# Kernel optimization log

Measured on AMD Instinct MI355X. Metric: run time of the kernel, lower is better.

The kernel has to match this reference:

```python
import jax, jax.numpy as jnp
import numpy as np

B, N, D = 4, 2048, 1024
HEAD_DIMS = 128
NUM_HEADS = 8
PROJ = HEAD_DIMS * NUM_HEADS  # 1024


def setup_inputs() -> dict:
    key = jax.random.key(0)
    ks = jax.random.split(key, 5)
    # Weights stored as (in, out); xavier-normal-like scale
    def xavier(k, fan_in, fan_out):
        std = (2.0 / (fan_in + fan_out)) ** 0.5
        return jax.random.normal(k, (fan_in, fan_out), dtype=jnp.float32) * std
    return {
        "x": jax.random.normal(ks[0], (B, N, D), dtype=jnp.float32),
        "Wq": xavier(ks[1], D, PROJ),
        "Wk": xavier(ks[2], D, PROJ),
        "Wv": xavier(ks[3], D, PROJ),
        "Wo": xavier(ks[4], PROJ, PROJ),
    }


def reference(x, Wq, Wk, Wv, Wo):
    b, n, d = x.shape
    # QKV projections, split into heads: (b, h, n, hd)
    def split_heads(z):
        return z.reshape(b, n, NUM_HEADS, HEAD_DIMS).transpose(0, 2, 1, 3)
    q = split_heads(x @ Wq)
    k = split_heads(x @ Wk)
    v = split_heads(x @ Wv)
    scale = 1.0 / jnp.sqrt(jnp.float32(HEAD_DIMS))
    logits = jnp.einsum("bhqd,bhkd->bhqk", q, k) * scale
    weights = jax.nn.softmax(logits, axis=-1)
    out = jnp.einsum("bhqk,bhkd->bhqd", weights, v)
    out = out.transpose(0, 2, 1, 3).reshape(b, n, PROJ)
    return out @ Wo
```

## Files before the change

### kernel.cpp

```cpp
#include <hip/hip_runtime.h>
#include <hip/hip_bf16.h>


typedef __attribute__((ext_vector_type(8))) short short8;
typedef __attribute__((ext_vector_type(4))) short short4v;
typedef __attribute__((ext_vector_type(4))) float floatx4;
typedef __attribute__((ext_vector_type(8))) _Float16 half8;

#define MFMA_F16(a, b, c) __builtin_amdgcn_mfma_f32_16x16x32_f16( \
    __builtin_bit_cast(half8, (a)), __builtin_bit_cast(half8, (b)), (c), 0, 0, 0)

static constexpr int BATCH  = 4;
static constexpr int NHEADS = 8;
static constexpr int SEQ    = 2048;
static constexpr int HD     = 128;
static constexpr int DMODEL = 1024;
static constexpr int MROWS  = BATCH * SEQ;
static constexpr int NQKV   = 3 * DMODEL;

#define QSCALE2 0.12752283786512624f

static __device__ __forceinline__ short f16bits(float v) {
    return __builtin_bit_cast(short, (_Float16)v);
}

template <typename T>
static __device__ __forceinline__ short8 load8_f16(const T* p) {
    if constexpr (sizeof(T) == 2) {
        return *(const short8*)p;
    } else {
        const float4 f0 = *(const float4*)p;
        const float4 f1 = *(const float4*)(p + 4);
        short8 r;
        r[0] = f16bits(f0.x); r[1] = f16bits(f0.y);
        r[2] = f16bits(f0.z); r[3] = f16bits(f0.w);
        r[4] = f16bits(f1.x); r[5] = f16bits(f1.y);
        r[6] = f16bits(f1.z); r[7] = f16bits(f1.w);
        return r;
    }
}

static __device__ __forceinline__ void storeC(float* C, size_t idx, float v) {
    C[idx] = v;
}
static __device__ __forceinline__ void storeC(_Float16* C, size_t idx, float v) {
    C[idx] = (_Float16)v;
}

static __device__ __forceinline__ void gload16(const short* g, short* l) {
    __builtin_amdgcn_global_load_lds(
        (const __attribute__((address_space(1))) void*)g,
        (__attribute__((address_space(3))) void*)l, 16, 0, 0);
}

__global__ __launch_bounds__(256)
void prep(const float* __restrict__ x, short* __restrict__ xb,
          const float* __restrict__ W0, const float* __restrict__ W1,
          const float* __restrict__ W2, const float* __restrict__ W3,
          short* __restrict__ Wt, int K, int N)
{
    __shared__ short T[32][33];
    const int z = blockIdx.z;
    if (z >= 4) {
        const size_t chunk = ((size_t)(z - 4) * 1024 + blockIdx.y * 32 + blockIdx.x);
        const size_t i = (chunk * 256 + threadIdx.x) * 8;
        *(short8*)&xb[i] = load8_f16(&x[i]);
        return;
    }
    const float* W = (z == 0) ? W0 : (z == 1) ? W1 : (z == 2) ? W2 : W3;
    short* Wtz = Wt + (size_t)z * K * N;

    const int n0 = blockIdx.x * 32, k0 = blockIdx.y * 32;
    const int r = threadIdx.x >> 3, c4 = (threadIdx.x & 7) * 4;

    const float4 v = *(const float4*)&W[(size_t)(k0 + r) * N + n0 + c4];
    T[r][c4 + 0] = f16bits(v.x);
    T[r][c4 + 1] = f16bits(v.y);
    T[r][c4 + 2] = f16bits(v.z);
    T[r][c4 + 3] = f16bits(v.w);
    __syncthreads();

    short4v o;
    o[0] = T[c4 + 0][r]; o[1] = T[c4 + 1][r];
    o[2] = T[c4 + 2][r]; o[3] = T[c4 + 3][r];
    *(short4v*)&Wtz[(size_t)(n0 + r) * K + k0 + c4] = o;
}

__global__ __launch_bounds__(256)
void convx(const float* __restrict__ x, short* __restrict__ xb)
{
    const size_t i = ((size_t)blockIdx.x * 256 + threadIdx.x) * 8;
    *(short8*)&xb[i] = load8_f16(&x[i]);
}

__global__ __launch_bounds__(256)
void transpose_v(const short* __restrict__ V, short* __restrict__ Vt)
{
    __shared__ short T[64][72];
    const int s0 = blockIdx.x * 64;
    const int d0 = blockIdx.y * 64;
    const int bh = blockIdx.z;
    const short* Vi = V  + (size_t)bh * SEQ * HD;
    short*       Vo = Vt + (size_t)bh * HD * SEQ;

    const int r = threadIdx.x >> 3;
    const int c = threadIdx.x & 7;

    *(short8*)&T[r][c * 8]      = *(const short8*)&Vi[(size_t)(s0 + r) * HD + d0 + c * 8];
    *(short8*)&T[r + 32][c * 8] = *(const short8*)&Vi[(size_t)(s0 + r + 32) * HD + d0 + c * 8];
    __syncthreads();

    short8 o0, o1;
    #pragma unroll
    for (int j = 0; j < 8; ++j) {
        o0[j] = T[c * 8 + j][r];
        o1[j] = T[c * 8 + j][r + 32];
    }
    *(short8*)&Vo[(size_t)(d0 + r) * SEQ + s0 + c * 8]      = o0;
    *(short8*)&Vo[(size_t)(d0 + r + 32) * SEQ + s0 + c * 8] = o1;
}

template <typename OutT, bool QKV>
__global__ __launch_bounds__(256)
void gemm128(const short* __restrict__ A, const short* __restrict__ Bt,
             OutT* __restrict__ C, int M, int N, int K, size_t qkvStride)
{
    __shared__ __align__(16) short As[128 * 64];
    __shared__ __align__(16) short Bs[128 * 64];

    const int tid  = threadIdx.x;
    const int lane = tid & 63;
    const int w    = tid >> 6;
    const int quad = lane >> 4;
    const int l16  = lane & 15;

    const int m0 = blockIdx.x * 128;
    const int n0 = blockIdx.y * 128;
    const int wm = (w >> 1) * 64;
    const int wn = (w & 1) * 64;

    floatx4 acc[4][4] = {};

    const int srow   = tid >> 3;
    const int schunk = (tid & 7) ^ (srow & 7);
    const short* aG = A  + (size_t)(m0 + srow) * K + schunk * 8;
    const short* bG = Bt + (size_t)(n0 + srow) * K + schunk * 8;
    short* aL = As + tid * 8;
    short* bL = Bs + tid * 8;

    const int fsw = l16 & 7;

    for (int k0 = 0; k0 < K; k0 += 64) {
        __syncthreads();
        #pragma unroll
        for (int r = 0; r < 4; ++r) {
            gload16(aG + k0 + (size_t)(r * 32) * K, aL + r * 2048);
            gload16(bG + k0 + (size_t)(r * 32) * K, bL + r * 2048);
        }
        __syncthreads();

        #pragma unroll
        for (int kk = 0; kk < 2; ++kk) {
            short8 af[4], bf[4];
            #pragma unroll
            for (int mi = 0; mi < 4; ++mi)
                af[mi] = *(short8*)&As[(wm + mi * 16 + l16) * 64 +
                                       (((kk * 4 + quad) ^ fsw) * 8)];
            #pragma unroll
            for (int ni = 0; ni < 4; ++ni)
                bf[ni] = *(short8*)&Bs[(wn + ni * 16 + l16) * 64 +
                                       (((kk * 4 + quad) ^ fsw) * 8)];

            #pragma unroll
            for (int mi = 0; mi < 4; ++mi)
                #pragma unroll
                for (int ni = 0; ni < 4; ++ni)
                    acc[mi][ni] = MFMA_F16(af[mi], bf[ni], acc[mi][ni]);
        }
    }

    #pragma unroll
    for (int mi = 0; mi < 4; ++mi)
        #pragma unroll
        for (int ni = 0; ni < 4; ++ni)
            #pragma unroll
            for (int r = 0; r < 4; ++r) {
                const int m = m0 + wm + mi * 16 + quad * 4 + r;
                const int n = n0 + wn + ni * 16 + l16;
                float v = acc[mi][ni][r];
                if constexpr (QKV) {
                    const int qkv = n >> 10, rem = n & 1023;
                    const int h = rem >> 7, d = rem & 127;
                    const int b = m >> 11, s = m & 2047;
                    if (qkv == 0) v *= QSCALE2;
                    storeC(C, (size_t)qkv * qkvStride +
                              (((size_t)b * NHEADS + h) * SEQ + s) * HD + d, v);
                } else {
                    storeC(C, (size_t)m * N + n, v);
                }
            }
}

__global__ __launch_bounds__(256)
void attn_flash10(const short* __restrict__ Q, const short* __restrict__ K,
                  const short* __restrict__ Vt, _Float16* __restrict__ O)
{
    __shared__ __align__(16) short Ks[2][32 * 128];
    __shared__ __align__(16) short Vs[2][128 * 32];
    __shared__ __align__(16) short Plds[4][16 * 40];

    const int tid  = threadIdx.x;
    const int lane = tid & 63;
    const int w    = tid >> 6;
    const int quad = lane >> 4;
    const int l16  = lane & 15;

    const int h  = blockIdx.x & 7;
    const int qi = blockIdx.x >> 3;
    const int b  = blockIdx.y;
    const int q0 = qi * 64;

    const short* Qh  = Q  + (((size_t)b * NHEADS + h) * SEQ) * HD;
    const short* Kh  = K  + (((size_t)b * NHEADS + h) * SEQ) * HD;
    const short* Vth = Vt + (((size_t)b * NHEADS + h) * HD) * SEQ;

    const int qrow = q0 + w * 16 + l16;
    short8 qf[4];
    #pragma unroll
    for (int c = 0; c < 4; ++c)
        qf[c] = *(const short8*)&Qh[(size_t)qrow * HD + c * 32 + quad * 8];

    const int kr0 = tid >> 4, kc0 = tid & 15;
    const int kr1 = kr0 + 16;
    const short* kGa = Kh + (size_t)kr0 * HD + ((kc0 ^ (kr0 & 15)) * 8);
    const short* kGb = Kh + (size_t)kr1 * HD + ((kc0 ^ (kr1 & 15)) * 8);
    const int vr0 = tid >> 2, vp0 = tid & 3;
    const short* vGa = Vth + (size_t)vr0 * SEQ + ((vp0 ^ ((vr0 >> 1) & 3)) * 8);
    const short* vGb = Vth + (size_t)(vr0 + 64) * SEQ + ((vp0 ^ ((vr0 >> 1) & 3)) * 8);

    floatx4 acc[8] = {};
    floatx4 acc9 = {};

    short8 ones;
    #pragma unroll
    for (int j = 0; j < 8; ++j) ones[j] = 0x3C00;

    const int fswV = (l16 >> 1) & 3;
    short* Pw = &Plds[w][0];

    auto STAGE = [&](short* kDst, short* vDst, int tile) {
        const size_t ko = (size_t)tile * 32 * HD;
        const size_t vo = (size_t)tile * 32;
        gload16(kGa + ko, kDst + tid * 8);
        gload16(kGb + ko, kDst + (tid + 256) * 8);
        gload16(vGa + vo, vDst + tid * 8);
        gload16(vGb + vo, vDst + (tid + 256) * 8);
    };

    auto COMPUTE = [&](const short* Kb, const short* Vb) {
        floatx4 s0 = {}, s1 = {};
        #pragma unroll
        for (int c = 0; c < 4; ++c) {
            const int k_ = c * 4 + quad;
            short8 kf0 = *(short8*)&Kb[l16 * 128 + ((k_ ^ l16) * 8)];
            short8 kf1 = *(short8*)&Kb[(16 + l16) * 128 + ((k_ ^ l16) * 8)];
            s0 = MFMA_F16(qf[c], kf0, s0);
            s1 = MFMA_F16(qf[c], kf1, s1);
        }
        #pragma unroll
        for (int r = 0; r < 4; ++r) {
            const float p0 = __builtin_amdgcn_exp2f(s0[r]);
            const float p1 = __builtin_amdgcn_exp2f(s1[r]);
            Pw[(quad * 4 + r) * 40 + l16]      = f16bits(p0);
            Pw[(quad * 4 + r) * 40 + 16 + l16] = f16bits(p1);
        }
        short8 pf = *(short8*)&Pw[l16 * 40 + quad * 8];
        acc9 = MFMA_F16(pf, ones, acc9);
        #pragma unroll
        for (int hc = 0; hc < 8; ++hc) {
            short8 vf = *(short8*)&Vb[(hc * 16 + l16) * 32 + ((quad ^ fswV) * 8)];
            acc[hc] = MFMA_F16(pf, vf, acc[hc]);
        }
    };

    STAGE(&Ks[0][0], &Vs[0][0], 0);

    for (int kt = 0; kt < SEQ; kt += 64) {
        const int t = kt >> 5;
        __syncthreads();
        STAGE(&Ks[1][0], &Vs[1][0], t + 1);
        COMPUTE(&Ks[0][0], &Vs[0][0]);
        __syncthreads();
        if (kt + 64 < SEQ)
            STAGE(&Ks[0][0], &Vs[0][0], t + 2);
        COMPUTE(&Ks[1][0], &Vs[1][0]);
    }

    float rinv[4];
    #pragma unroll
    for (int r = 0; r < 4; ++r)
        rinv[r] = 1.0f / fmaxf(acc9[r], 1e-30f);

    #pragma unroll
    for (int hc = 0; hc < 8; ++hc)
        #pragma unroll
        for (int r = 0; r < 4; ++r) {
            const int row = q0 + w * 16 + quad * 4 + r;
            O[((size_t)b * SEQ + row) * DMODEL + h * HD + hc * 16 + l16] =
                (_Float16)(acc[hc][r] * rinv[r]);
        }
}

template <typename AT, typename OutT>
__global__ __launch_bounds__(256)
void gemm64(const AT* __restrict__ A, const float* __restrict__ W,
            OutT* __restrict__ C, int M, int N, int K, int headsplit)
{
    __shared__ __align__(16) short As[64][32];
    __shared__ __align__(16) short Bs[64][32];

    const int tid  = threadIdx.x;
    const int lane = tid & 63;
    const int w    = tid >> 6;
    const int quad = lane >> 4;
    const int l16  = lane & 15;

    const int m0 = blockIdx.x * 64;
    const int n0 = blockIdx.y * 64;
    const int wm = (w >> 1) * 32;
    const int wn = (w & 1) * 32;

    floatx4 acc[2][2] = {};

    const int arow = tid >> 2, acol = (tid & 3) * 8;
    const int brow = tid >> 3, bcol = (tid & 7) * 8;

    const AT*    aptr = A + (size_t)(m0 + arow) * K + acol;
    const float* bptr = W + (size_t)brow * N + n0 + bcol;

    for (int k0 = 0; k0 < K; k0 += 32) {
        short8 av = load8_f16(aptr + k0);
        short8 bv = load8_f16(bptr + (size_t)k0 * N);
        __syncthreads();
        *(short8*)&As[arow][acol] = av;
        #pragma unroll
        for (int j = 0; j < 8; ++j)
            Bs[bcol + j][brow] = bv[j];
        __syncthreads();

        short8 af0 = *(short8*)&As[wm + l16][quad * 8];
        short8 af1 = *(short8*)&As[wm + 16 + l16][quad * 8];
        short8 bf0 = *(short8*)&Bs[wn + l16][quad * 8];
        short8 bf1 = *(short8*)&Bs[wn + 16 + l16][quad * 8];

        acc[0][0] = MFMA_F16(af0, bf0, acc[0][0]);
        acc[0][1] = MFMA_F16(af0, bf1, acc[0][1]);
        acc[1][0] = MFMA_F16(af1, bf0, acc[1][0]);
        acc[1][1] = MFMA_F16(af1, bf1, acc[1][1]);
    }

    #pragma unroll
    for (int mi = 0; mi < 2; ++mi)
        #pragma unroll
        for (int ni = 0; ni < 2; ++ni)
            #pragma unroll
            for (int r = 0; r < 4; ++r) {
                const int m = m0 + wm + mi * 16 + quad * 4 + r;
                const int n = n0 + wn + ni * 16 + l16;
                const float v = acc[mi][ni][r];
                if (headsplit) {
                    const int b = m >> 11, nn = m & 2047;
                    const int h = n >> 7,  d  = n & 127;
                    storeC(C, (((size_t)b * NHEADS + h) * SEQ + nn) * HD + d, v);
                } else {
                    storeC(C, (size_t)m * N + n, v);
                }
            }
}

__global__ __launch_bounds__(256)
void attn_flash(const short* __restrict__ Q, const short* __restrict__ K,
                const short* __restrict__ V, _Float16* __restrict__ O)
{
    __shared__ __align__(16) short Ksf[32][136];
    __shared__ __align__(16) short Vtl[HD][40];
    __shared__ __align__(16) short Pldsf[4][16][40];

    const int tid  = threadIdx.x;
    const int lane = tid & 63;
    const int w    = tid >> 6;
    const int quad = lane >> 4;
    const int l16  = lane & 15;

    const int q0 = blockIdx.x * 64;
    const int h  = blockIdx.y;
    const int b  = blockIdx.z;

    const size_t headoff = ((size_t)b * NHEADS + h) * SEQ * HD;
    const short* Qh = Q + headoff;
    const short* Kh = K + headoff;
    const short* Vh = V + headoff;

    const float scale = 0.08838834764831845f;

    const int qrow = q0 + w * 16 + l16;
    short8 qf[4];
    #pragma unroll
    for (int c = 0; c < 4; ++c)
        qf[c] = *(const short8*)&Qh[(size_t)qrow * HD + c * 32 + quad * 8];

    float mrow[4], lrow[4];
    #pragma unroll
    for (int r = 0; r < 4; ++r) { mrow[r] = -1e30f; lrow[r] = 0.f; }
    floatx4 acc[8] = {};

    const int krow = tid >> 4, kcol = (tid & 15) * 8;
    const int vkey = tid & 31;
    const int vhd  = (tid >> 5) * 16;

    for (int kt = 0; kt < SEQ; kt += 32) {
        const short* Kt = Kh + (size_t)kt * HD;
        short8 k0v = *(const short8*)(Kt + (size_t)tid * 8);
        short8 k1v = *(const short8*)(Kt + (size_t)(tid + 256) * 8);
        short8 v0 = *(const short8*)&Vh[(size_t)(kt + vkey) * HD + vhd];
        short8 v1 = *(const short8*)&Vh[(size_t)(kt + vkey) * HD + vhd + 8];

        __syncthreads();
        *(short8*)&Ksf[krow][kcol]      = k0v;
        *(short8*)&Ksf[krow + 16][kcol] = k1v;
        #pragma unroll
        for (int j = 0; j < 8; ++j) {
            Vtl[vhd + j][vkey]     = v0[j];
            Vtl[vhd + 8 + j][vkey] = v1[j];
        }
        __syncthreads();

        floatx4 s0 = {}, s1 = {};
        #pragma unroll
        for (int c = 0; c < 4; ++c) {
            short8 kf0 = *(short8*)&Ksf[l16][c * 32 + quad * 8];
            short8 kf1 = *(short8*)&Ksf[16 + l16][c * 32 + quad * 8];
            s0 = MFMA_F16(qf[c], kf0, s0);
            s1 = MFMA_F16(qf[c], kf1, s1);
        }

        float p0[4], p1[4], alpha[4];
        #pragma unroll
        for (int r = 0; r < 4; ++r) {
            const float a  = s0[r] * scale;
            const float bb = s1[r] * scale;
            float mx = fmaxf(a, bb);
            mx = fmaxf(mx, __shfl_xor(mx, 1));
            mx = fmaxf(mx, __shfl_xor(mx, 2));
            mx = fmaxf(mx, __shfl_xor(mx, 4));
            mx = fmaxf(mx, __shfl_xor(mx, 8));
            const float mnew = fmaxf(mrow[r], mx);
            alpha[r] = __expf(mrow[r] - mnew);
            mrow[r]  = mnew;
            p0[r] = __expf(a - mnew);
            p1[r] = __expf(bb - mnew);
            float rs = p0[r] + p1[r];
            rs += __shfl_xor(rs, 1);
            rs += __shfl_xor(rs, 2);
            rs += __shfl_xor(rs, 4);
            rs += __shfl_xor(rs, 8);
            lrow[r] = lrow[r] * alpha[r] + rs;
        }
        #pragma unroll
        for (int hc = 0; hc < 8; ++hc)
            #pragma unroll
            for (int r = 0; r < 4; ++r)
                acc[hc][r] *= alpha[r];

        #pragma unroll
        for (int r = 0; r < 4; ++r) {
            Pldsf[w][quad * 4 + r][l16]      = f16bits(p0[r]);
            Pldsf[w][quad * 4 + r][16 + l16] = f16bits(p1[r]);
        }
        __syncthreads();

        short8 pf = *(short8*)&Pldsf[w][l16][quad * 8];
        #pragma unroll
        for (int hc = 0; hc < 8; ++hc) {
            short8 vf = *(short8*)&Vtl[hc * 16 + l16][quad * 8];
            acc[hc] = MFMA_F16(pf, vf, acc[hc]);
        }
    }

    #pragma unroll
    for (int hc = 0; hc < 8; ++hc)
        #pragma unroll
        for (int r = 0; r < 4; ++r) {
            const int row = q0 + w * 16 + quad * 4 + r;
            const float val = acc[hc][r] / fmaxf(lrow[r], 1e-30f);
            O[((size_t)b * SEQ + row) * DMODEL + h * HD + hc * 16 + l16] =
                (_Float16)val;
        }
}

extern "C" void kernel_launch(void* const* d_in, const int* in_sizes, int n_in,
                              void* d_out, int out_size, void* d_ws, size_t ws_size,
                              hipStream_t stream)
{
    const float* x  = (const float*)d_in[0];
    const float* Wq = (const float*)d_in[1];
    const float* Wk = (const float*)d_in[2];
    const float* Wv = (const float*)d_in[3];
    const float* Wo = (const float*)d_in[4];
    float* out = (float*)d_out;

    const size_t bufElems = (size_t)MROWS * DMODEL;
    const size_t batElems = (size_t)SEQ * DMODEL;
    const size_t MiB = 1024 * 1024;
    dim3 tt(256);

    if (ws_size >= 72 * MiB) {
        short* xb    = (short*)d_ws;
        short* Qb    = xb + bufElems;
        short* Kb    = xb + 2 * bufElems;
        short* Vn    = xb + 3 * bufElems;
        short* Wtall = xb + 4 * bufElems;
        short* Wto   = Wtall + 3 * (size_t)DMODEL * DMODEL;
        short* VtG   = xb;
        short* Ab    = Vn;

        prep<<<dim3(32, 32, 8), tt, 0, stream>>>(
            x, xb, Wq, Wk, Wv, Wo, Wtall, DMODEL, DMODEL);

        gemm128<_Float16, true><<<dim3(MROWS / 128, NQKV / 128), tt, 0, stream>>>(
            xb, Wtall, (_Float16*)Qb, MROWS, NQKV, DMODEL, bufElems);

        transpose_v<<<dim3(SEQ / 64, HD / 64, BATCH * NHEADS), tt, 0, stream>>>(Vn, VtG);

        attn_flash10<<<dim3(NHEADS * (SEQ / 64), BATCH), tt, 0, stream>>>(
            Qb, Kb, VtG, (_Float16*)Ab);

        gemm128<float, false><<<dim3(MROWS / 128, DMODEL / 128), tt, 0, stream>>>(
            Ab, Wto, out, MROWS, DMODEL, DMODEL, 0);
    } else if (ws_size >= 64 * MiB) {
        short* xb    = (short*)d_ws;
        short* Qb    = xb + 2 * batElems;
        short* Kb    = Qb + 4 * batElems;
        short* Vn    = Kb + 4 * batElems;
        short* Wtall = Vn + 4 * batElems;
        short* Wto   = Wtall + 3 * (size_t)DMODEL * DMODEL;

        prep<<<dim3(32, 32, 4), tt, 0, stream>>>(
            nullptr, nullptr, Wq, Wk, Wv, Wo, Wtall, DMODEL, DMODEL);

        for (int half = 0; half < 2; ++half) {
            const size_t off = (size_t)half * 2 * batElems;
            convx<<<dim3(2048), tt, 0, stream>>>(x + off, xb);
            gemm128<_Float16, true><<<dim3(32, NQKV / 128), tt, 0, stream>>>(
                xb, Wtall, (_Float16*)(Qb + off), 2 * SEQ, NQKV, DMODEL,
                4 * batElems);
        }
        for (int half = 0; half < 2; ++half) {
            const size_t off = (size_t)half * 2 * batElems;
            transpose_v<<<dim3(SEQ / 64, HD / 64, 2 * NHEADS), tt, 0, stream>>>(
                Vn + off, xb);
            attn_flash10<<<dim3(NHEADS * (SEQ / 64), 2), tt, 0, stream>>>(
                Qb + off, Kb + off, xb, (_Float16*)(Vn + off));
        }
        gemm128<float, false><<<dim3(MROWS / 128, DMODEL / 128), tt, 0, stream>>>(
            Vn, Wto, out, MROWS, DMODEL, DMODEL, 0);
    } else if (ws_size >= 24 * MiB) {
        short* xb    = (short*)d_ws;
        short* Qb    = xb + batElems;
        short* Kb    = xb + 2 * batElems;
        short* Vb    = xb + 3 * batElems;
        short* Wtall = xb + 4 * batElems;
        short* Wto   = Wtall + 3 * (size_t)DMODEL * DMODEL;

        prep<<<dim3(32, 32, 4), tt, 0, stream>>>(
            nullptr, nullptr, Wq, Wk, Wv, Wo, Wtall, DMODEL, DMODEL);

        for (int b = 0; b < BATCH; ++b) {
            convx<<<dim3(1024), tt, 0, stream>>>(x + (size_t)b * batElems, xb);
            gemm128<_Float16, true><<<dim3(SEQ / 128, NQKV / 128), tt, 0, stream>>>(
                xb, Wtall, (_Float16*)Qb, SEQ, NQKV, DMODEL, batElems);
            transpose_v<<<dim3(SEQ / 64, HD / 64, NHEADS), tt, 0, stream>>>(Vb, xb);
            attn_flash10<<<dim3(NHEADS * (SEQ / 64), 1), tt, 0, stream>>>(
                Qb, Kb, xb, (_Float16*)Vb);
            gemm128<float, false><<<dim3(SEQ / 128, DMODEL / 128), tt, 0, stream>>>(
                Vb, Wto, out + (size_t)b * batElems, SEQ, DMODEL, DMODEL, 0);
        }
    } else {
        short* Qb = (short*)d_ws;
        short* Kb = Qb + batElems;
        short* Vb = Qb + 2 * batElems;
        short* Ab = Qb + 3 * batElems;

        dim3 gg(SEQ / 64, DMODEL / 64);
        for (int b = 0; b < BATCH; ++b) {
            const float* xb_ = x + (size_t)b * batElems;
            gemm64<float, _Float16><<<gg, tt, 0, stream>>>(
                xb_, Wq, (_Float16*)Qb, SEQ, DMODEL, DMODEL, 1);
            gemm64<float, _Float16><<<gg, tt, 0, stream>>>(
                xb_, Wk, (_Float16*)Kb, SEQ, DMODEL, DMODEL, 1);
            gemm64<float, _Float16><<<gg, tt, 0, stream>>>(
                xb_, Wv, (_Float16*)Vb, SEQ, DMODEL, DMODEL, 1);
            attn_flash<<<dim3(SEQ / 64, NHEADS, 1), tt, 0, stream>>>(
                Qb, Kb, Vb, (_Float16*)Ab);
            gemm64<short, float><<<gg, tt, 0, stream>>>(
                Ab, Wo, out + (size_t)b * batElems, SEQ, DMODEL, DMODEL, 0);
        }
    }
}
```

Before: 290.9 us.

## Give each attention wave two 16-row query tiles to reuse K/V fragments

Result: no change. 291.3 us (+0.1%).

```diff
diff --git a/kernel.cpp b/kernel.cpp
--- a/kernel.cpp
+++ b/kernel.cpp
@@ -201,13 +201,13 @@
             }
 }
 
-__global__ __launch_bounds__(256)
-void attn_flash10(const short* __restrict__ Q, const short* __restrict__ K,
+__global__ __launch_bounds__(128)
+void attn_flash11(const short* __restrict__ Q, const short* __restrict__ K,
                   const short* __restrict__ Vt, _Float16* __restrict__ O)
 {
     __shared__ __align__(16) short Ks[2][32 * 128];
     __shared__ __align__(16) short Vs[2][128 * 32];
-    __shared__ __align__(16) short Plds[4][16 * 40];
+    __shared__ __align__(16) short Plds[2][32 * 40];
 
     const int tid  = threadIdx.x;
     const int lane = tid & 63;
@@ -224,22 +224,23 @@
     const short* Kh  = K  + (((size_t)b * NHEADS + h) * SEQ) * HD;
     const short* Vth = Vt + (((size_t)b * NHEADS + h) * HD) * SEQ;
 
-    const int qrow = q0 + w * 16 + l16;
-    short8 qf[4];
-    #pragma unroll
-    for (int c = 0; c < 4; ++c)
-        qf[c] = *(const short8*)&Qh[(size_t)qrow * HD + c * 32 + quad * 8];
+    short8 qf[2][4];
+    #pragma unroll
+    for (int mi = 0; mi < 2; ++mi) {
+        const int qrow = q0 + w * 32 + mi * 16 + l16;
+        #pragma unroll
+        for (int c = 0; c < 4; ++c)
+            qf[mi][c] = *(const short8*)&Qh[(size_t)qrow * HD + c * 32 + quad * 8];
+    }
 
     const int kr0 = tid >> 4, kc0 = tid & 15;
-    const int kr1 = kr0 + 16;
-    const short* kGa = Kh + (size_t)kr0 * HD + ((kc0 ^ (kr0 & 15)) * 8);
-    const short* kGb = Kh + (size_t)kr1 * HD + ((kc0 ^ (kr1 & 15)) * 8);
+    const short* kA0 = Kh + (size_t)kr0 * HD + ((kc0 ^ kr0) * 8);
+    const short* kA1 = Kh + (size_t)(kr0 + 8) * HD + ((kc0 ^ (kr0 + 8)) * 8);
     const int vr0 = tid >> 2, vp0 = tid & 3;
-    const short* vGa = Vth + (size_t)vr0 * SEQ + ((vp0 ^ ((vr0 >> 1) & 3)) * 8);
-    const short* vGb = Vth + (size_t)(vr0 + 64) * SEQ + ((vp0 ^ ((vr0 >> 1) & 3)) * 8);
-
-    floatx4 acc[8] = {};
-    floatx4 acc9 = {};
+    const short* vA = Vth + (size_t)vr0 * SEQ + ((vp0 ^ ((vr0 >> 1) & 3)) * 8);
+
+    floatx4 acc[2][8] = {};
+    floatx4 acc9[2] = {};
 
     short8 ones;
     #pragma unroll
@@ -251,35 +252,51 @@
     auto STAGE = [&](short* kDst, short* vDst, int tile) {
         const size_t ko = (size_t)tile * 32 * HD;
         const size_t vo = (size_t)tile * 32;
-        gload16(kGa + ko, kDst + tid * 8);
-        gload16(kGb + ko, kDst + (tid + 256) * 8);
-        gload16(vGa + vo, vDst + tid * 8);
-        gload16(vGb + vo, vDst + (tid + 256) * 8);
+        gload16(kA0 + ko,            kDst + tid * 8);
+        gload16(kA1 + ko,            kDst + (tid + 128) * 8);
+        gload16(kA0 + ko + 16 * HD,  kDst + (tid + 256) * 8);
+        gload16(kA1 + ko + 16 * HD,  kDst + (tid + 384) * 8);
+        gload16(vA + vo,                        vDst + tid * 8);
+        gload16(vA + vo + (size_t)32 * SEQ,     vDst + (tid + 128) * 8);
+        gload16(vA + vo + (size_t)64 * SEQ,     vDst + (tid + 256) * 8);
+        gload16(vA + vo + (size_t)96 * SEQ,     vDst + (tid + 384) * 8);
     };
 
     auto COMPUTE = [&](const short* Kb, const short* Vb) {
-        floatx4 s0 = {}, s1 = {};
+        floatx4 s[2][2] = {};
         #pragma unroll
         for (int c = 0; c < 4; ++c) {
             const int k_ = c * 4 + quad;
             short8 kf0 = *(short8*)&Kb[l16 * 128 + ((k_ ^ l16) * 8)];
             short8 kf1 = *(short8*)&Kb[(16 + l16) * 128 + ((k_ ^ l16) * 8)];
-            s0 = MFMA_F16(qf[c], kf0, s0);
-            s1 = MFMA_F16(qf[c], kf1, s1);
-        }
-        #pragma unroll
-        for (int r = 0; r < 4; ++r) {
-            const float p0 = __builtin_amdgcn_exp2f(s0[r]);
-            const float p1 = __builtin_amdgcn_exp2f(s1[r]);
-            Pw[(quad * 4 + r) * 40 + l16]      = f16bits(p0);
-            Pw[(quad * 4 + r) * 40 + 16 + l16] = f16bits(p1);
-        }
-        short8 pf = *(short8*)&Pw[l16 * 40 + quad * 8];
-        acc9 = MFMA_F16(pf, ones, acc9);
+            #pragma unroll
+            for (int mi = 0; mi < 2; ++mi) {
+                s[mi][0] = MFMA_F16(qf[mi][c], kf0, s[mi][0]);
+                s[mi][1] = MFMA_F16(qf[mi][c], kf1, s[mi][1]);
+            }
+        }
+        #pragma unroll
+        for (int mi = 0; mi < 2; ++mi)
+            #pragma unroll
+            for (int r = 0; r < 4; ++r) {
+                const float p0 = __builtin_amdgcn_exp2f(s[mi][0][r]);
+                const float p1 = __builtin_amdgcn_exp2f(s[mi][1][r]);
+                const int prow = mi * 16 + quad * 4 + r;
+                Pw[prow * 40 + l16]      = f16bits(p0);
+                Pw[prow * 40 + 16 + l16] = f16bits(p1);
+            }
+        short8 pf[2];
+        #pragma unroll
+        for (int mi = 0; mi < 2; ++mi) {
+            pf[mi] = *(short8*)&Pw[(mi * 16 + l16) * 40 + quad * 8];
+            acc9[mi] = MFMA_F16(pf[mi], ones, acc9[mi]);
+        }
         #pragma unroll
         for (int hc = 0; hc < 8; ++hc) {
             short8 vf = *(short8*)&Vb[(hc * 16 + l16) * 32 + ((quad ^ fswV) * 8)];
-            acc[hc] = MFMA_F16(pf, vf, acc[hc]);
+            #pragma unroll
+            for (int mi = 0; mi < 2; ++mi)
+                acc[mi][hc] = MFMA_F16(pf[mi], vf, acc[mi][hc]);
         }
     };
 
@@ -296,19 +313,21 @@
         COMPUTE(&Ks[1][0], &Vs[1][0]);
     }
 
-    float rinv[4];
-    #pragma unroll
-    for (int r = 0; r < 4; ++r)
-        rinv[r] = 1.0f / fmaxf(acc9[r], 1e-30f);
-
-    #pragma unroll
-    for (int hc = 0; hc < 8; ++hc)
-        #pragma unroll
-        for (int r = 0; r < 4; ++r) {
-            const int row = q0 + w * 16 + quad * 4 + r;
-            O[((size_t)b * SEQ + row) * DMODEL + h * HD + hc * 16 + l16] =
-                (_Float16)(acc[hc][r] * rinv[r]);
-        }
+    #pragma unroll
+    for (int mi = 0; mi < 2; ++mi) {
+        float rinv[4];
+        #pragma unroll
+        for (int r = 0; r < 4; ++r)
+            rinv[r] = 1.0f / fmaxf(acc9[mi][r], 1e-30f);
+        #pragma unroll
+        for (int hc = 0; hc < 8; ++hc)
+            #pragma unroll
+            for (int r = 0; r < 4; ++r) {
+                const int row = q0 + w * 32 + mi * 16 + quad * 4 + r;
+                O[((size_t)b * SEQ + row) * DMODEL + h * HD + hc * 16 + l16] =
+                    (_Float16)(acc[mi][hc][r] * rinv[r]);
+            }
+    }
 }
 
 template <typename AT, typename OutT>
@@ -513,6 +532,7 @@
     const size_t batElems = (size_t)SEQ * DMODEL;
     const size_t MiB = 1024 * 1024;
     dim3 tt(256);
+    dim3 ta(128);
 
     if (ws_size >= 72 * MiB) {
         short* xb    = (short*)d_ws;
@@ -532,7 +552,7 @@
 
         transpose_v<<<dim3(SEQ / 64, HD / 64, BATCH * NHEADS), tt, 0, stream>>>(Vn, VtG);
 
-        attn_flash10<<<dim3(NHEADS * (SEQ / 64), BATCH), tt, 0, stream>>>(
+        attn_flash11<<<dim3(NHEADS * (SEQ / 64), BATCH), ta, 0, stream>>>(
             Qb, Kb, VtG, (_Float16*)Ab);
 
         gemm128<float, false><<<dim3(MROWS / 128, DMODEL / 128), tt, 0, stream>>>(
@@ -559,7 +579,7 @@
             const size_t off = (size_t)half * 2 * batElems;
             transpose_v<<<dim3(SEQ / 64, HD / 64, 2 * NHEADS), tt, 0, stream>>>(
                 Vn + off, xb);
-            attn_flash10<<<dim3(NHEADS * (SEQ / 64), 2), tt, 0, stream>>>(
+            attn_flash11<<<dim3(NHEADS * (SEQ / 64), 2), ta, 0, stream>>>(
                 Qb + off, Kb + off, xb, (_Float16*)(Vn + off));
         }
         gemm128<float, false><<<dim3(MROWS / 128, DMODEL / 128), tt, 0, stream>>>(
@@ -580,7 +600,7 @@
             gemm128<_Float16, true><<<dim3(SEQ / 128, NQKV / 128), tt, 0, stream>>>(
                 xb, Wtall, (_Float16*)Qb, SEQ, NQKV, DMODEL, batElems);
             transpose_v<<<dim3(SEQ / 64, HD / 64, NHEADS), tt, 0, stream>>>(Vb, xb);
-            attn_flash10<<<dim3(NHEADS * (SEQ / 64), 1), tt, 0, stream>>>(
+            attn_flash11<<<dim3(NHEADS * (SEQ / 64), 1), ta, 0, stream>>>(
                 Qb, Kb, xb, (_Float16*)Vb);
             gemm128<float, false><<<dim3(SEQ / 128, DMODEL / 128), tt, 0, stream>>>(
                 Vb, Wto, out + (size_t)b * batElems, SEQ, DMODEL, DMODEL, 0);
```
